# Kernel tuning notes

Hardware: AMD Instinct MI355X
Metric: run time of the kernel (lower is better)

Reference implementation:

```python
import jax, jax.numpy as jnp
import numpy as np

B, N, H, E = 8, 2048, 4, 64  # batch, nodes, heads, embedding_dim (= GAT out_channels)
NEG_SLOPE = 0.2


def setup_inputs() -> dict:
    key = jax.random.key(0)
    ks = jax.random.split(key, 12)
    state = jax.random.normal(ks[0], (B, N), dtype=jnp.float32)
    strucEmb = jax.random.normal(ks[1], (N, E), dtype=jnp.float32) * 0.1
    # adjacency mask: True where NO edge (masked_fill -inf). Keep self-loops so every row has an edge.
    no_edge = jax.random.uniform(ks[2], (N, N)) > 0.02
    adj_mask = no_edge.at[jnp.arange(N), jnp.arange(N)].set(False)
    g = lambda k, shp: jax.random.normal(k, shp, dtype=jnp.float32) * np.float32(np.sqrt(2.0 / sum(shp[-2:])))
    W_gat = g(ks[3], (1, H * E))          # torch Linear(1, H*E, bias=False) weight.T laid out as (in,out)
    att = g(ks[4], (H, 2 * E, 1))         # GAT additive attention params
    Ws = g(ks[5], (E, E))                 # weight_struc (out,in)
    Wst = g(ks[6], (E, E))                # weight_state (out,in)
    lin1_w = g(ks[7], (E, E)); lin1_b = jnp.zeros((E,), jnp.float32)
    lin2_w = g(ks[8], (E, E)); lin2_b = jnp.zeros((E,), jnp.float32)
    lin3_w = g(ks[9], (1, 2 * E)); lin3_b = jnp.zeros((1,), jnp.float32)
    return dict(state=state, strucEmb=strucEmb, adj_mask=adj_mask, W_gat=W_gat, att=att,
                Ws=Ws, Wst=Wst, lin1_w=lin1_w, lin1_b=lin1_b, lin2_w=lin2_w, lin2_b=lin2_b,
                lin3_w=lin3_w, lin3_b=lin3_b)


def reference(state, strucEmb, adj_mask, W_gat, att, Ws, Wst,
              lin1_w, lin1_b, lin2_w, lin2_b, lin3_w, lin3_b):
    # --- Custom_GATConv_v2 ---
    # reshaped_state: [B,N,1]; Wh = state @ W -> [B,N,H*E] -> [B,H,N,E]
    Wh = (state[..., None] @ W_gat).reshape(B, N, H, E).transpose(0, 2, 1, 3)
    a_src = att[:, :E, 0]   # [H,E]
    a_tgt = att[:, E:, 0]   # [H,E]
    src = jnp.einsum('bhne,he->bhn', Wh, a_src)
    tgt = jnp.einsum('bhne,he->bhn', Wh, a_tgt)
    e = src[:, :, :, None] + tgt[:, :, None, :]          # [B,H,N,N]
    e = jnp.where(e > 0, e, NEG_SLOPE * e)               # LeakyReLU
    e = jnp.where(adj_mask[None, None], -jnp.inf, e)     # mask non-edges
    attn = jax.nn.softmax(e, axis=-1)
    x = jnp.einsum('bhij,bhje->bhie', attn, Wh).mean(axis=1)  # [B,N,E]

    # --- DeepQNet head (is_for_learn=True branch) ---
    x = jax.nn.relu(strucEmb @ Ws.T + x @ Wst.T)         # [B,N,E]
    state_emb = x.sum(axis=1)                            # [B,E]
    beta_state = state_emb @ lin1_w.T + lin1_b           # [B,E]
    beta_action = x @ lin2_w.T + lin2_b                  # [B,N,E]
    expand_state = jnp.broadcast_to(beta_state[:, None, :], (B, N, E))
    out = jax.nn.relu(jnp.concatenate([expand_state, beta_action], axis=2))  # [B,N,2E]
    return out @ lin3_w.T + lin3_b                       # [B,N,1]
```

## Files before the change

### kernel.cpp

```cpp
#include <hip/hip_runtime.h>

#define BB 8
#define NN 2048
#define HH 4
#define EE 64
#define MAXJ 128
#define NEG 0.2f
#define NCHUNK 32

static constexpr int OFF_CSRC  = 0;
static constexpr int OFF_CTGT  = 4;
static constexpr int OFF_WGWST = 8;
static constexpr int OFF_S     = 264;
static constexpr int OFF_SWS   = 288;
static constexpr int OFF_SATT  = OFF_SWS + NN * EE;
static constexpr int OFF_PART  = OFF_SATT + NN * 32;

__global__ __launch_bounds__(256) void k_prep(const float* __restrict__ W_gat,
                                              const float* __restrict__ att,
                                              const float* __restrict__ Wst,
                                              float* __restrict__ ws) {
    __shared__ float wg[HH * EE];
    int t = threadIdx.x;
    wg[t] = W_gat[t];
    __syncthreads();
    if (t < HH) {
        float cs = 0.f, ct = 0.f;
        for (int e = 0; e < EE; ++e) {
            cs += wg[t * EE + e] * att[t * 2 * EE + e];
            ct += wg[t * EE + e] * att[t * 2 * EE + EE + e];
        }
        ws[OFF_CSRC + t] = cs;
        ws[OFF_CTGT + t] = ct;
    }
    int h = t >> 6, f = t & 63;
    float acc = 0.f;
    for (int e = 0; e < EE; ++e) acc += wg[h * EE + e] * Wst[f * EE + e];
    ws[OFF_WGWST + t] = acc;
}

__global__ __launch_bounds__(256) void k_fsatt(const int* __restrict__ adj,
                                               const float* __restrict__ state,
                                               const float* __restrict__ strucEmb,
                                               const float* __restrict__ Ws,
                                               float* __restrict__ ws) {
    __shared__ float s_wsT[EE * 65];
    __shared__ int   s_jl[MAXJ];
    __shared__ int   s_cnt;
    __shared__ float s_y[BB * MAXJ];
    const int i = blockIdx.x;
    const int t = threadIdx.x;
    const int w = t >> 6, lane = t & 63;

    if (w == 0) {
        const int* a = adj + (size_t)i * NN;
        int cnt = 0;
        for (int it = 0; it < NN / 64; ++it) {
            int j = it * 64 + lane;
            bool edge = (a[j] == 0);
            unsigned long long m = __ballot(edge);
            if (edge) {
                int pos = cnt + __popcll(m & ((1ull << lane) - 1ull));
                if (pos < MAXJ) s_jl[pos] = j;
            }
            cnt += __popcll(m);
        }
        if (lane == 0) s_cnt = cnt > MAXJ ? MAXJ : cnt;
    } else if (w == 1) {
        for (int it = 0; it < EE; ++it)
            s_wsT[lane * 65 + it] = Ws[it * EE + lane];
    }
    __syncthreads();
    const int cnt = s_cnt;

    if (w == 0) {
        float v = strucEmb[(size_t)i * EE + lane];
        float acc = 0.f;
        for (int e = 0; e < EE; ++e)
            acc += __shfl(v, e) * s_wsT[e * 65 + lane];
        ws[OFF_SWS + i * EE + lane] = acc;
    } else {
        for (int x = t - 64; x < BB * MAXJ; x += 192) {
            int k = x & (MAXJ - 1);
            if (k < cnt) s_y[x] = state[(x >> 7) * NN + s_jl[k]];
        }
    }
    __syncthreads();

    int g = t >> 3, k0 = t & 7, b = g >> 2, h = g & 3;
    const float* yb = s_y + b * MAXJ;
    float ct = ws[OFF_CTGT + h];
    float si = state[b * NN + i] * ws[OFF_CSRC + h];
    float mmax = -1e30f;
    for (int k = k0; k < cnt; k += 8) {
        float e = si + ct * yb[k]; e = e > 0.f ? e : NEG * e;
        mmax = fmaxf(mmax, e);
    }
    for (int o = 4; o; o >>= 1) mmax = fmaxf(mmax, __shfl_xor(mmax, o, 8));
    float den = 0.f, num = 0.f;
    for (int k = k0; k < cnt; k += 8) {
        float y = yb[k];
        float e = si + ct * y; e = e > 0.f ? e : NEG * e;
        float p = expf(e - mmax);
        den += p; num += p * y;
    }
    for (int o = 4; o; o >>= 1) { den += __shfl_xor(den, o, 8); num += __shfl_xor(num, o, 8); }
    if (k0 == 0) ws[OFF_SATT + i * 32 + g] = num / den;
}

__global__ void k_se(float* __restrict__ ws) {
    int b = blockIdx.x & 7, chunk = blockIdx.x >> 3;
    int t = threadIdx.x;
    int f = t & 63, sl = t >> 6;
    float wgw[HH];
    for (int h = 0; h < HH; ++h) wgw[h] = 0.25f * ws[OFF_WGWST + h * EE + f];
    float acc = 0.f;
    int i0 = chunk * (NN / NCHUNK);
    for (int i = i0 + sl; i < i0 + NN / NCHUNK; i += 4) {
        float v = ws[OFF_SWS + i * EE + f];
        for (int h = 0; h < HH; ++h)
            v += ws[OFF_SATT + i * 32 + b * 4 + h] * wgw[h];
        acc += fmaxf(v, 0.f);
    }
    __shared__ float red[256];
    red[t] = acc;
    __syncthreads();
    if (t < EE)
        ws[OFF_PART + (size_t)blockIdx.x * EE + t] =
            red[t] + red[t + 64] + red[t + 128] + red[t + 192];
}

__global__ void k_S(const float* __restrict__ lin1_w, const float* __restrict__ lin1_b,
                    const float* __restrict__ lin3_w, const float* __restrict__ lin3_b,
                    float* __restrict__ ws) {
    int b = blockIdx.x;
    int t = threadIdx.x;
    __shared__ float s_l1T[EE * 65];
    __shared__ float s_se[EE];
    for (int it = 0; it < EE; ++it)
        s_l1T[t * 65 + it] = lin1_w[it * EE + t];
    float se = 0.f;
    for (int c = 0; c < NCHUNK; ++c)
        se += ws[OFF_PART + (size_t)(c * BB + b) * EE + t];
    s_se[t] = se;
    __syncthreads();
    float bs = lin1_b[t];
    for (int f2 = 0; f2 < EE; ++f2) bs += s_se[f2] * s_l1T[f2 * 65 + t];
    float r = fmaxf(bs, 0.f) * lin3_w[t];
    for (int o = 32; o; o >>= 1) r += __shfl_xor(r, o);
    if (t == 0) ws[OFF_S + b] = r + lin3_b[0];
}

__global__ __launch_bounds__(256) void k_out2(const float* __restrict__ lin2_w,
                                              const float* __restrict__ lin2_b,
                                              const float* __restrict__ lin3_w,
                                              const float* __restrict__ ws,
                                              float* __restrict__ out) {
    __shared__ float s_l2T[EE * 65];
    __shared__ float s_wgw[HH * EE];
    __shared__ float s_S[BB];
    __shared__ float s_l2b[EE], s_l3[EE];
    const int t = threadIdx.x;
    const int w = t >> 6, lane = t & 63;
    for (int k = t; k < EE * EE; k += 256) {
        int fp = k >> 6, f = k & 63;
        s_l2T[f * 65 + fp] = lin2_w[k];
    }
    s_wgw[t] = 0.25f * ws[OFF_WGWST + t];
    if (t < BB) s_S[t] = ws[OFF_S + t];
    if (t < EE) { s_l2b[t] = lin2_b[t]; s_l3[t] = lin3_w[EE + t]; }
    __syncthreads();

    const int i = blockIdx.x * 4 + w;
    float xsws = ws[OFF_SWS + i * EE + lane];
    float sa = (lane < 32) ? ws[OFF_SATT + i * 32 + lane] : 0.f;
    for (int b = 0; b < BB; ++b) {
        float xv = xsws;
        for (int h = 0; h < HH; ++h)
            xv += __shfl(sa, b * 4 + h) * s_wgw[h * EE + lane];
        xv = fmaxf(xv, 0.f);
        float acc = s_l2b[lane];
        for (int f = 0; f < EE; ++f) acc += __shfl(xv, f) * s_l2T[f * 65 + lane];
        float r = fmaxf(acc, 0.f) * s_l3[lane];
        for (int o = 32; o; o >>= 1) r += __shfl_xor(r, o);
        if (lane == 0) out[(size_t)b * NN + i] = s_S[b] + r;
    }
}

extern "C" void kernel_launch(void* const* d_in, const int* in_sizes, int n_in,
                              void* d_out, int out_size, void* d_ws, size_t ws_size,
                              hipStream_t stream) {
    const float* state    = (const float*)d_in[0];
    const float* strucEmb = (const float*)d_in[1];
    const int*   adj      = (const int*)d_in[2];
    const float* W_gat    = (const float*)d_in[3];
    const float* att      = (const float*)d_in[4];
    const float* Ws       = (const float*)d_in[5];
    const float* Wst      = (const float*)d_in[6];
    const float* lin1_w   = (const float*)d_in[7];
    const float* lin1_b   = (const float*)d_in[8];
    const float* lin2_w   = (const float*)d_in[9];
    const float* lin2_b   = (const float*)d_in[10];
    const float* lin3_w   = (const float*)d_in[11];
    const float* lin3_b   = (const float*)d_in[12];
    float* ws = (float*)d_ws;
    float* out = (float*)d_out;

    k_prep <<<dim3(1),           dim3(256), 0, stream>>>(W_gat, att, Wst, ws);
    k_fsatt<<<dim3(NN),          dim3(256), 0, stream>>>(adj, state, strucEmb, Ws, ws);
    k_se   <<<dim3(NCHUNK * BB), dim3(256), 0, stream>>>(ws);
    k_S    <<<dim3(BB),          dim3(64),  0, stream>>>(lin1_w, lin1_b, lin3_w, lin3_b, ws);
    k_out2 <<<dim3(NN / 4),      dim3(256), 0, stream>>>(lin2_w, lin2_b, lin3_w, ws, out);
}
```

Baseline: 52.11 us.

## Split strucEmb@Ws into own kernel and parallelize adjacency scan across warps

```diff
diff --git a/kernel.cpp b/kernel.cpp
--- a/kernel.cpp
+++ b/kernel.cpp
@@ -16,35 +16,51 @@
 static constexpr int OFF_SATT  = OFF_SWS + NN * EE;
 static constexpr int OFF_PART  = OFF_SATT + NN * 32;
 
-__global__ __launch_bounds__(256) void k_prep(const float* __restrict__ W_gat,
-                                              const float* __restrict__ att,
-                                              const float* __restrict__ Wst,
-                                              float* __restrict__ ws) {
-    __shared__ float wg[HH * EE];
-    int t = threadIdx.x;
-    wg[t] = W_gat[t];
-    __syncthreads();
-    if (t < HH) {
-        float cs = 0.f, ct = 0.f;
-        for (int e = 0; e < EE; ++e) {
-            cs += wg[t * EE + e] * att[t * 2 * EE + e];
-            ct += wg[t * EE + e] * att[t * 2 * EE + EE + e];
-        }
-        ws[OFF_CSRC + t] = cs;
-        ws[OFF_CTGT + t] = ct;
-    }
-    int h = t >> 6, f = t & 63;
-    float acc = 0.f;
-    for (int e = 0; e < EE; ++e) acc += wg[h * EE + e] * Wst[f * EE + e];
-    ws[OFF_WGWST + t] = acc;
+__global__ __launch_bounds__(256) void k_sws(const float* __restrict__ strucEmb,
+                                             const float* __restrict__ Ws,
+                                             const float* __restrict__ W_gat,
+                                             const float* __restrict__ att,
+                                             const float* __restrict__ Wst,
+                                             float* __restrict__ ws) {
+    __shared__ float s_wsT[EE * 65];
+    __shared__ float s_emb[16 * EE];
+    const int t = threadIdx.x;
+    const int w = t >> 6, lane = t & 63;
+    const int i0 = blockIdx.x * 16;
+    for (int k = t; k < EE * EE; k += 256)
+        s_wsT[(k & 63) * 65 + (k >> 6)] = Ws[k];
+    for (int k = t; k < 16 * EE; k += 256)
+        s_emb[k] = strucEmb[(size_t)i0 * EE + k];
+    __syncthreads();
+    for (int q = 0; q < 4; ++q) {
+        int r = w * 4 + q;
+        float v = s_emb[r * EE + lane];
+        float acc = 0.f;
+        for (int e = 0; e < EE; ++e)
+            acc += __shfl(v, e) * s_wsT[e * 65 + lane];
+        ws[OFF_SWS + (size_t)(i0 + r) * EE + lane] = acc;
+    }
+    if (blockIdx.x == 0) {
+        int h = t >> 6, f = t & 63;
+        float acc = 0.f;
+        for (int e = 0; e < EE; ++e) acc += W_gat[h * EE + e] * Wst[f * EE + e];
+        ws[OFF_WGWST + t] = acc;
+        if (t < 2 * HH) {
+            int hh = t & 3;
+            const float* wgx = W_gat + hh * EE;
+            const float* av  = att + hh * 2 * EE + (t >= HH ? EE : 0);
+            float a2 = 0.f;
+            for (int e = 0; e < EE; ++e) a2 += wgx[e] * av[e];
+            if (t < HH) ws[OFF_CSRC + hh] = a2; else ws[OFF_CTGT + hh] = a2;
+        }
+    }
 }
 
 __global__ __launch_bounds__(256) void k_fsatt(const int* __restrict__ adj,
                                                const float* __restrict__ state,
-                                               const float* __restrict__ strucEmb,
-                                               const float* __restrict__ Ws,
                                                float* __restrict__ ws) {
-    __shared__ float s_wsT[EE * 65];
+    __shared__ int   s_jq[4][MAXJ];
+    __shared__ int   s_c[4];
     __shared__ int   s_jl[MAXJ];
     __shared__ int   s_cnt;
     __shared__ float s_y[BB * MAXJ];
@@ -52,38 +68,47 @@
     const int t = threadIdx.x;
     const int w = t >> 6, lane = t & 63;
 
-    if (w == 0) {
-        const int* a = adj + (size_t)i * NN;
-        int cnt = 0;
-        for (int it = 0; it < NN / 64; ++it) {
-            int j = it * 64 + lane;
-            bool edge = (a[j] == 0);
-            unsigned long long m = __ballot(edge);
-            if (edge) {
-                int pos = cnt + __popcll(m & ((1ull << lane) - 1ull));
-                if (pos < MAXJ) s_jl[pos] = j;
-            }
-            cnt += __popcll(m);
-        }
-        if (lane == 0) s_cnt = cnt > MAXJ ? MAXJ : cnt;
-    } else if (w == 1) {
-        for (int it = 0; it < EE; ++it)
-            s_wsT[lane * 65 + it] = Ws[it * EE + lane];
+    {
+        const int4* a4 = (const int4*)(adj + (size_t)i * NN) + w * 128;
+        int base = 0;
+        const unsigned long long below = (1ull << lane) - 1ull;
+        for (int q = 0; q < 2; ++q) {
+            int4 v = a4[q * 64 + lane];
+            int j0 = w * 512 + (q * 64 + lane) * 4;
+            int eb = (v.x == 0 ? 1 : 0) | (v.y == 0 ? 2 : 0) |
+                     (v.z == 0 ? 4 : 0) | (v.w == 0 ? 8 : 0);
+            unsigned long long b0 = __ballot(eb & 1), b1 = __ballot(eb & 2);
+            unsigned long long b2 = __ballot(eb & 4), b3 = __ballot(eb & 8);
+            int pos = base + __popcll(b0 & below) + __popcll(b1 & below)
+                           + __popcll(b2 & below) + __popcll(b3 & below);
+            if (eb & 1) { if (pos < MAXJ) s_jq[w][pos] = j0 + 0; ++pos; }
+            if (eb & 2) { if (pos < MAXJ) s_jq[w][pos] = j0 + 1; ++pos; }
+            if (eb & 4) { if (pos < MAXJ) s_jq[w][pos] = j0 + 2; ++pos; }
+            if (eb & 8) { if (pos < MAXJ) s_jq[w][pos] = j0 + 3; ++pos; }
+            base += __popcll(b0) + __popcll(b1) + __popcll(b2) + __popcll(b3);
+        }
+        if (lane == 0) s_c[w] = base > MAXJ ? MAXJ : base;
+    }
+    __syncthreads();
+    {
+        int start = 0;
+        for (int q = 0; q < w; ++q) start += s_c[q];
+        int cw = s_c[w];
+        for (int k = lane; k < cw; k += 64) {
+            int p = start + k;
+            if (p < MAXJ) s_jl[p] = s_jq[w][k];
+        }
+        if (t == 0) {
+            int tot = s_c[0] + s_c[1] + s_c[2] + s_c[3];
+            s_cnt = tot > MAXJ ? MAXJ : tot;
+        }
     }
     __syncthreads();
     const int cnt = s_cnt;
 
-    if (w == 0) {
-        float v = strucEmb[(size_t)i * EE + lane];
-        float acc = 0.f;
-        for (int e = 0; e < EE; ++e)
-            acc += __shfl(v, e) * s_wsT[e * 65 + lane];
-        ws[OFF_SWS + i * EE + lane] = acc;
-    } else {
-        for (int x = t - 64; x < BB * MAXJ; x += 192) {
-            int k = x & (MAXJ - 1);
-            if (k < cnt) s_y[x] = state[(x >> 7) * NN + s_jl[k]];
-        }
+    for (int x = t; x < BB * MAXJ; x += 256) {
+        int k = x & (MAXJ - 1);
+        if (k < cnt) s_y[x] = state[(x >> 7) * NN + s_jl[k]];
     }
     __syncthreads();
 
@@ -206,8 +231,8 @@
     float* ws = (float*)d_ws;
     float* out = (float*)d_out;
 
-    k_prep <<<dim3(1),           dim3(256), 0, stream>>>(W_gat, att, Wst, ws);
-    k_fsatt<<<dim3(NN),          dim3(256), 0, stream>>>(adj, state, strucEmb, Ws, ws);
+    k_sws  <<<dim3(NN / 16),     dim3(256), 0, stream>>>(strucEmb, Ws, W_gat, att, Wst, ws);
+    k_fsatt<<<dim3(NN),          dim3(256), 0, stream>>>(adj, state, ws);
     k_se   <<<dim3(NCHUNK * BB), dim3(256), 0, stream>>>(ws);
     k_S    <<<dim3(BB),          dim3(64),  0, stream>>>(lin1_w, lin1_b, lin3_w, lin3_b, ws);
     k_out2 <<<dim3(NN / 4),      dim3(256), 0, stream>>>(lin2_w, lin2_b, lin3_w, ws, out);
```

Measured after the change: 48.29 us. 7.3% less time.
